# Kernel tuning notes

Measured on AMD Instinct MI355X. Metric: run time of the kernel, lower is better.

Reference implementation:

```python
import jax, jax.numpy as jnp
import numpy as np

N = 100000
E = 3200000
D = 64  # in_feats == hidden_feats == 64 (hardcoded in module)


def setup_inputs() -> dict:
    key = jax.random.key(0)
    ks = jax.random.split(key, 12)
    s = 1.0 / np.sqrt(D)
    return {
        "x": jax.random.normal(ks[0], (N, D), dtype=jnp.float32),
        "edge_index": jax.random.randint(ks[1], (2, E), 0, N, dtype=jnp.int64),
        "W1": jax.random.uniform(ks[2], (D, D), jnp.float32, -s, s),
        "b1": jnp.zeros((D,), jnp.float32),
        "W2": jax.random.uniform(ks[3], (D, D), jnp.float32, -s, s),
        "b2": jnp.zeros((D,), jnp.float32),
        "Wq": jax.random.uniform(ks[4], (D, D), jnp.float32, -s, s),
        "bq": jax.random.uniform(ks[5], (D,), jnp.float32, -s, s),
        "Wk": jax.random.uniform(ks[6], (D, D), jnp.float32, -s, s),
        "bk": jax.random.uniform(ks[7], (D,), jnp.float32, -s, s),
        "Wv": jax.random.uniform(ks[8], (D, D), jnp.float32, -s, s),
        "bv": jax.random.uniform(ks[9], (D,), jnp.float32, -s, s),
    }


def gcn_conv(x, src, dst, deg_inv_sqrt, W, b):
    # PyG GCNConv: linear -> normalized scatter-add over edges (self-loops included in src/dst)
    h = x @ W  # [N, D]
    norm = deg_inv_sqrt[src] * deg_inv_sqrt[dst]  # [E+N]
    msg = h[src] * norm[:, None]  # gather + scale
    out = jax.ops.segment_sum(msg, dst, num_segments=x.shape[0])  # scatter-add
    return out + b


def reference(x, edge_index, W1, b1, W2, b2, Wq, bq, Wk, bk, Wv, bv):
    n = x.shape[0]
    loop = jnp.arange(n, dtype=edge_index.dtype)
    src = jnp.concatenate([edge_index[0], loop])
    dst = jnp.concatenate([edge_index[1], loop])
    deg = jax.ops.segment_sum(jnp.ones_like(src, dtype=x.dtype), dst, num_segments=n)
    deg_inv_sqrt = jnp.where(deg > 0, jax.lax.rsqrt(deg), 0.0)

    h = jax.nn.relu(gcn_conv(x, src, dst, deg_inv_sqrt, W1, b1))
    # dropout with training=False -> identity; F.relu(relu(h)) == relu(h)
    h = jax.nn.relu(gcn_conv(h, src, dst, deg_inv_sqrt, W2, b2))

    # Attention with seq_len == 1
    q = h @ Wq + bq  # [N, D]
    k = h @ Wk + bk
    v = h @ Wv + bv
    scores = jnp.sum(q * k, axis=-1, keepdims=True)[:, :, None]  # [N,1,1]
    att = jax.nn.softmax(scores, axis=-1)  # == 1 for seq_len 1, kept for faithfulness
    context = att * v[:, None, :]  # [N,1,D]
    return context
```

## Files before the change

kernel.cpp:

```cpp
#include <hip/hip_runtime.h>
#include <hip/hip_bf16.h>
#include <cstdint>
#include <cstddef>


#define BN_SHIFT 8
#define BN 256
#define NBK 512
#define PCHUNK 4096
#define PCAP 16
#define BCAP 10240

static __device__ __forceinline__ uint32_t f32_to_bf16_bits(float f) {
    uint32_t u = __builtin_bit_cast(uint32_t, f);
    u += 0x7fffu + ((u >> 16) & 1u);
    return u >> 16;
}

static __device__ __forceinline__ void add_bf16x8(float* acc, uint4 q) {
    uint32_t w0 = q.x, w1 = q.y, w2 = q.z, w3 = q.w;
    acc[0] += __builtin_bit_cast(float, w0 << 16);
    acc[1] += __builtin_bit_cast(float, w0 & 0xffff0000u);
    acc[2] += __builtin_bit_cast(float, w1 << 16);
    acc[3] += __builtin_bit_cast(float, w1 & 0xffff0000u);
    acc[4] += __builtin_bit_cast(float, w2 << 16);
    acc[5] += __builtin_bit_cast(float, w2 & 0xffff0000u);
    acc[6] += __builtin_bit_cast(float, w3 << 16);
    acc[7] += __builtin_bit_cast(float, w3 & 0xffff0000u);
}

__global__ __launch_bounds__(256) void hist_kernel(const int* __restrict__ ei,
                                                   int* __restrict__ pcnt, int E) {
    __shared__ int lc[NBK];
    int tid = threadIdx.x;
    lc[tid] = 0; lc[tid + 256] = 0;
    __syncthreads();

    int e0 = blockIdx.x * PCHUNK;
    int m = min(PCHUNK, E - e0);
    const int* dsts = ei + E + e0;
    if ((((uintptr_t)dsts) & 15) == 0) {
        int m4 = m >> 2;
        for (int t = tid; t < m4; t += 256) {
            int4 d = ((const int4*)dsts)[t];
            atomicAdd(&lc[d.x >> BN_SHIFT], 1);
            atomicAdd(&lc[d.y >> BN_SHIFT], 1);
            atomicAdd(&lc[d.z >> BN_SHIFT], 1);
            atomicAdd(&lc[d.w >> BN_SHIFT], 1);
        }
        for (int i = (m4 << 2) + tid; i < m; i += 256)
            atomicAdd(&lc[dsts[i] >> BN_SHIFT], 1);
    } else {
        for (int i = tid; i < m; i += 256)
            atomicAdd(&lc[dsts[i] >> BN_SHIFT], 1);
    }
    __syncthreads();
    int* row = pcnt + (size_t)blockIdx.x * NBK;
    row[tid] = lc[tid];
    row[tid + 256] = lc[tid + 256];
}

__global__ __launch_bounds__(256) void pscan_kernel(int* __restrict__ pcnt,
                                                    int* __restrict__ bcnt, int PB) {
    __shared__ int ss[256];
    int b = blockIdx.x;
    int tid = threadIdx.x;
    int iper = (PB + 255) >> 8;
    int i0 = tid * iper;
    int i1 = min(PB, i0 + iper);
    int vals[8];
    int s = 0;
    for (int i = i0, k = 0; i < i1; ++i, ++k) {
        vals[k] = pcnt[(size_t)i * NBK + b];
        s += vals[k];
    }
    ss[tid] = s;
    __syncthreads();
    for (int o = 1; o < 256; o <<= 1) {
        int u = (tid >= o) ? ss[tid - o] : 0;
        __syncthreads();
        ss[tid] += u;
        __syncthreads();
    }
    int run = ss[tid] - s;
    for (int i = i0, k = 0; i < i1; ++i, ++k) {
        pcnt[(size_t)i * NBK + b] = run;
        run += vals[k];
    }
    if (tid == 255) bcnt[b] = ss[255];
}

__global__ __launch_bounds__(256) void bscan_kernel(const int* __restrict__ bcnt,
                                                    int* __restrict__ bbase) {
    __shared__ int s[256];
    int t = threadIdx.x;
    int c0 = bcnt[2 * t], c1 = bcnt[2 * t + 1];
    int v = c0 + c1;
    s[t] = v;
    __syncthreads();
    for (int off = 1; off < 256; off <<= 1) {
        int u = (t >= off) ? s[t - off] : 0;
        __syncthreads();
        s[t] += u;
        __syncthreads();
    }
    int ex = s[t] - v;
    bbase[2 * t] = ex;
    bbase[2 * t + 1] = ex + c0;
    if (t == 255) bbase[NBK] = ex + c0 + c1;
}

__global__ __launch_bounds__(256) void part_kernel(const int* __restrict__ ei,
                                                   const int* __restrict__ bbase,
                                                   const int* __restrict__ poff,
                                                   uint32_t* __restrict__ stage, int E) {
    __shared__ int cnt[NBK];
    __shared__ int base[NBK];
    __shared__ uint32_t bins[NBK * PCAP];
    int tid = threadIdx.x;
    cnt[tid] = 0; cnt[tid + 256] = 0;
    {
        const int* prow = poff + (size_t)blockIdx.x * NBK;
        base[tid] = bbase[tid] + prow[tid];
        base[tid + 256] = bbase[tid + 256] + prow[tid + 256];
    }
    __syncthreads();

    int e0 = blockIdx.x * PCHUNK;
#pragma unroll
    for (int k = 0; k < PCHUNK / 256; ++k) {
        int e = e0 + (k << 8) + tid;
        if (e < E) {
            int s = ei[e];
            int d = ei[E + e];
            int b = d >> BN_SHIFT;
            uint32_t pack = (uint32_t)s | ((uint32_t)(d & (BN - 1)) << 17);
            int pos = atomicAdd(&cnt[b], 1);
            if (pos < PCAP) bins[b * PCAP + pos] = pack;
            else stage[base[b] + pos] = pack;
        }
    }
    __syncthreads();

    int wave = tid >> 6, lane = tid & 63;
    int sub = lane >> 4, idx = lane & 15;
    for (int b0 = wave * 4; b0 < NBK; b0 += 16) {
        int b = b0 + sub;
        int c = min(cnt[b], PCAP);
        if (idx < c) stage[base[b] + idx] = bins[b * PCAP + idx];
    }
}

__global__ __launch_bounds__(256) void build_kernel(const uint32_t* __restrict__ stage,
                                                    const int* __restrict__ bbase,
                                                    int* __restrict__ rowptr,
                                                    float* __restrict__ dis,
                                                    int* __restrict__ col, int n) {
    __shared__ uint32_t eb[BCAP];
    __shared__ int cnt[BN];
    __shared__ int off[BN];
    __shared__ int cur[BN];
    __shared__ int ssum[256];
    int tid = threadIdx.x;
    int b = blockIdx.x;
    int node0 = b << BN_SHIFT;
    int ebase = bbase[b];
    int ecnt = bbase[b + 1] - ebase;
    int colbase = ebase + node0;

    cnt[tid] = 0;
    cur[tid] = 0;
    __syncthreads();

    bool fits = (ecnt <= BCAP);
    for (int i = tid; i < ecnt; i += 256) {
        uint32_t pk = stage[ebase + i];
        if (fits) eb[i] = pk;
        atomicAdd(&cnt[pk >> 17], 1);
    }
    __syncthreads();

    int c = cnt[tid] + 1;
    ssum[tid] = c;
    __syncthreads();
    for (int o = 1; o < 256; o <<= 1) {
        int u = (tid >= o) ? ssum[tid - o] : 0;
        __syncthreads();
        ssum[tid] += u;
        __syncthreads();
    }
    int ex = ssum[tid] - c;
    off[tid] = ex;
    int node = node0 + tid;
    if (node <= n) rowptr[node] = colbase + ex;
    if (node < n) {
        dis[node] = rsqrtf((float)c);
        col[colbase + ex] = node << 7;
    }
    __syncthreads();

    if (fits) {
        for (int i = tid; i < ecnt; i += 256) {
            uint32_t pk = eb[i];
            int doff = pk >> 17;
            int p = atomicAdd(&cur[doff], 1);
            col[colbase + off[doff] + 1 + p] = (int)(pk & 0x1ffff) << 7;
        }
    } else {
        for (int i = tid; i < ecnt; i += 256) {
            uint32_t pk = stage[ebase + i];
            int doff = pk >> 17;
            int p = atomicAdd(&cur[doff], 1);
            col[colbase + off[doff] + 1 + p] = (int)(pk & 0x1ffff) << 7;
        }
    }
}

template <int MODE>
__global__ __launch_bounds__(256) void gemm_kernel(const float* __restrict__ x,
                                                   const float* __restrict__ W,
                                                   const float* __restrict__ dis,
                                                   const float* __restrict__ bias,
                                                   void* __restrict__ out, int n) {
    __shared__ float Wl[64 * 64];
    int t = threadIdx.x;
    {
        const float4* W4 = (const float4*)W;
        float4* Wl4 = (float4*)Wl;
#pragma unroll
        for (int i = 0; i < 4; ++i) Wl4[t + i * 256] = W4[t + i * 256];
    }
    __syncthreads();

    int row = blockIdx.x * 256 + t;
    if (row >= n) return;

    const float4* xr = (const float4*)(x + (size_t)row * 64);
    float4 acc4[16];
#pragma unroll
    for (int p = 0; p < 16; ++p) acc4[p] = make_float4(0.f, 0.f, 0.f, 0.f);

    float4 xq = xr[0];
    for (int k4 = 0; k4 < 16; ++k4) {
        float4 xn = xq;
        if (k4 < 15) xn = xr[k4 + 1];
        float xs[4] = {xq.x, xq.y, xq.z, xq.w};
#pragma unroll
        for (int kk = 0; kk < 4; ++kk) {
            float xk = xs[kk];
            const float4* wr = (const float4*)&Wl[((k4 << 2) + kk) << 6];
#pragma unroll
            for (int j4 = 0; j4 < 16; ++j4) {
                float4 wv = wr[j4];
                acc4[j4].x = fmaf(xk, wv.x, acc4[j4].x);
                acc4[j4].y = fmaf(xk, wv.y, acc4[j4].y);
                acc4[j4].z = fmaf(xk, wv.z, acc4[j4].z);
                acc4[j4].w = fmaf(xk, wv.w, acc4[j4].w);
            }
        }
        xq = xn;
    }

    if (MODE == 0) {
        float s = dis[row];
        uint4* go = (uint4*)out;
#pragma unroll
        for (int p = 0; p < 8; ++p) {
            float4 a = acc4[2 * p];
            float4 bq = acc4[2 * p + 1];
            uint4 o;
            o.x = (f32_to_bf16_bits(a.y * s) << 16) | f32_to_bf16_bits(a.x * s);
            o.y = (f32_to_bf16_bits(a.w * s) << 16) | f32_to_bf16_bits(a.z * s);
            o.z = (f32_to_bf16_bits(bq.y * s) << 16) | f32_to_bf16_bits(bq.x * s);
            o.w = (f32_to_bf16_bits(bq.w * s) << 16) | f32_to_bf16_bits(bq.z * s);
            go[(size_t)row * 8 + p] = o;
        }
    } else {
        const float4* b4 = (const float4*)bias;
        float4* fo = (float4*)out;
#pragma unroll
        for (int p = 0; p < 16; ++p) {
            float4 bb = b4[p];
            float4 a = acc4[p];
            a.x += bb.x; a.y += bb.y; a.z += bb.z; a.w += bb.w;
            fo[(size_t)row * 16 + p] = a;
        }
    }
}

__global__ __launch_bounds__(256) void agg_kernel(const char* __restrict__ g,
                                                  const int* __restrict__ rowptr,
                                                  const int* __restrict__ col,
                                                  const float* __restrict__ dis,
                                                  const float* __restrict__ bias,
                                                  float* __restrict__ out, int n) {
    int wid = (blockIdx.x * 256 + threadIdx.x) >> 6;
    if (wid >= n) return;
    int lane = threadIdx.x & 63;
    int grp = lane >> 3;
    int chk16 = (lane & 7) << 4;

    float acc[8];
#pragma unroll
    for (int j = 0; j < 8; ++j) acc[j] = 0.f;

    int beg = rowptr[wid];
    int end = rowptr[wid + 1];
    int e = beg + grp;
    for (; e + 8 < end; e += 16) {
        int o0 = col[e] + chk16;
        int o1 = col[e + 8] + chk16;
        uint4 q0 = *(const uint4*)(g + o0);
        uint4 q1 = *(const uint4*)(g + o1);
        add_bf16x8(acc, q0);
        add_bf16x8(acc, q1);
    }
    if (e < end) {
        int o = col[e] + chk16;
        add_bf16x8(acc, *(const uint4*)(g + o));
    }

#pragma unroll
    for (int m = 8; m < 64; m <<= 1) {
#pragma unroll
        for (int j = 0; j < 8; ++j) acc[j] += __shfl_xor(acc[j], m, 64);
    }

    float dv = dis[wid];
    float v = acc[0];
#pragma unroll
    for (int j = 1; j < 8; ++j) v = (grp == j) ? acc[j] : v;
    int f = (chk16 >> 1) + grp;
    v = fmaxf(fmaf(v, dv, bias[f]), 0.f);
    out[(size_t)wid * 64 + f] = v;
}

extern "C" void kernel_launch(void* const* d_in, const int* in_sizes, int n_in,
                              void* d_out, int out_size, void* d_ws, size_t ws_size,
                              hipStream_t stream) {
    const float* x  = (const float*)d_in[0];
    const int*   ei = (const int*)d_in[1];
    const float* W1 = (const float*)d_in[2];
    const float* b1 = (const float*)d_in[3];
    const float* W2 = (const float*)d_in[4];
    const float* b2 = (const float*)d_in[5];
    const float* Wv = (const float*)d_in[10];
    const float* bv = (const float*)d_in[11];

    const int N = in_sizes[0] / 64;
    const int E = in_sizes[1] / 2;
    const int NB = (N + BN - 1) >> BN_SHIFT;
    const int PB = (E + PCHUNK - 1) / PCHUNK;

    auto align_up = [](size_t v) { return (v + 255) & ~(size_t)255; };
    char* p = (char*)d_ws;
    int*   rowptr = (int*)p;    p += align_up((size_t)(N + 1) * 4);
    float* dis    = (float*)p;  p += align_up((size_t)N * 4);
    int*   pcnt   = (int*)p;    p += align_up((size_t)PB * NBK * 4);
    int*   bcnt   = (int*)p;    p += align_up((size_t)NBK * 4);
    int*   bbase  = (int*)p;    p += align_up((size_t)(NBK + 1) * 4);
    int*   col    = (int*)p;    p += align_up((size_t)(E + N + BN) * 4);
    size_t gsz    = (size_t)N * 128 > (size_t)E * 4 ? (size_t)N * 128 : (size_t)E * 4;
    char*  gbuf   = p;          p += align_up(gsz);
    float* xbuf   = (float*)p;  p += align_up((size_t)N * 256);
    uint32_t* stage = (uint32_t*)gbuf;

    int nbl = (N + 255) / 256;
    int abl = (N + 3) / 4;

    hist_kernel<<<PB, 256, 0, stream>>>(ei, pcnt, E);
    pscan_kernel<<<NBK, 256, 0, stream>>>(pcnt, bcnt, PB);
    bscan_kernel<<<1, 256, 0, stream>>>(bcnt, bbase);
    part_kernel<<<PB, 256, 0, stream>>>(ei, bbase, pcnt, stage, E);
    build_kernel<<<NB, 256, 0, stream>>>(stage, bbase, rowptr, dis, col, N);

    gemm_kernel<0><<<nbl, 256, 0, stream>>>(x, W1, dis, nullptr, gbuf, N);
    agg_kernel<<<abl, 256, 0, stream>>>(gbuf, rowptr, col, dis, b1, xbuf, N);

    gemm_kernel<0><<<nbl, 256, 0, stream>>>(xbuf, W2, dis, nullptr, gbuf, N);
    agg_kernel<<<abl, 256, 0, stream>>>(gbuf, rowptr, col, dis, b2, xbuf, N);

    gemm_kernel<1><<<nbl, 256, 0, stream>>>(xbuf, Wv, nullptr, bv, d_out, N);
}
```

Before: 350.8 us.

## Map one 8-lane group per node in aggregation and fold block scan into consumers

The aggregation kernel now assigns each node to an 8-lane group that walks all of its edges serially, instead of spreading a node's edges across a full wave. This removes the cross-lane shuffle reduction and lets each wave hold eight nodes' gathers in flight, and outputs are written as float4. Separately, the single-block bucket scan kernel is removed and the scan is recomputed redundantly inside each partition and build block, saving one launch at the cost of extra per-block work. Lanes may sit idle when node degrees differ within a wave.

```diff
diff --git a/kernel.cpp b/kernel.cpp
--- a/kernel.cpp
+++ b/kernel.cpp
@@ -27,6 +27,26 @@
     acc[5] += __builtin_bit_cast(float, w2 & 0xffff0000u);
     acc[6] += __builtin_bit_cast(float, w3 << 16);
     acc[7] += __builtin_bit_cast(float, w3 & 0xffff0000u);
+}
+
+static __device__ __forceinline__ void scan_bcnt(const int* __restrict__ bcnt,
+                                                 int* sbb, int* ssum) {
+    int t = threadIdx.x;
+    int c0 = bcnt[2 * t], c1 = bcnt[2 * t + 1];
+    int v = c0 + c1;
+    ssum[t] = v;
+    __syncthreads();
+    for (int o = 1; o < 256; o <<= 1) {
+        int u = (t >= o) ? ssum[t - o] : 0;
+        __syncthreads();
+        ssum[t] += u;
+        __syncthreads();
+    }
+    int ex = ssum[t] - v;
+    sbb[2 * t] = ex;
+    sbb[2 * t + 1] = ex + c0;
+    if (t == 255) sbb[NBK] = ex + c0 + c1;
+    __syncthreads();
 }
 
 __global__ __launch_bounds__(256) void hist_kernel(const int* __restrict__ ei,
@@ -90,39 +110,23 @@
     if (tid == 255) bcnt[b] = ss[255];
 }
 
-__global__ __launch_bounds__(256) void bscan_kernel(const int* __restrict__ bcnt,
-                                                    int* __restrict__ bbase) {
-    __shared__ int s[256];
-    int t = threadIdx.x;
-    int c0 = bcnt[2 * t], c1 = bcnt[2 * t + 1];
-    int v = c0 + c1;
-    s[t] = v;
-    __syncthreads();
-    for (int off = 1; off < 256; off <<= 1) {
-        int u = (t >= off) ? s[t - off] : 0;
-        __syncthreads();
-        s[t] += u;
-        __syncthreads();
-    }
-    int ex = s[t] - v;
-    bbase[2 * t] = ex;
-    bbase[2 * t + 1] = ex + c0;
-    if (t == 255) bbase[NBK] = ex + c0 + c1;
-}
-
 __global__ __launch_bounds__(256) void part_kernel(const int* __restrict__ ei,
-                                                   const int* __restrict__ bbase,
+                                                   const int* __restrict__ bcnt,
                                                    const int* __restrict__ poff,
                                                    uint32_t* __restrict__ stage, int E) {
+    __shared__ int sbb[NBK + 1];
+    __shared__ int ssum[256];
     __shared__ int cnt[NBK];
     __shared__ int base[NBK];
     __shared__ uint32_t bins[NBK * PCAP];
     int tid = threadIdx.x;
+    scan_bcnt(bcnt, sbb, ssum);
+
     cnt[tid] = 0; cnt[tid + 256] = 0;
     {
         const int* prow = poff + (size_t)blockIdx.x * NBK;
-        base[tid] = bbase[tid] + prow[tid];
-        base[tid + 256] = bbase[tid + 256] + prow[tid + 256];
+        base[tid] = sbb[tid] + prow[tid];
+        base[tid + 256] = sbb[tid + 256] + prow[tid + 256];
     }
     __syncthreads();
 
@@ -152,20 +156,22 @@
 }
 
 __global__ __launch_bounds__(256) void build_kernel(const uint32_t* __restrict__ stage,
-                                                    const int* __restrict__ bbase,
+                                                    const int* __restrict__ bcnt,
                                                     int* __restrict__ rowptr,
                                                     float* __restrict__ dis,
                                                     int* __restrict__ col, int n) {
+    __shared__ int sbb[NBK + 1];
     __shared__ uint32_t eb[BCAP];
     __shared__ int cnt[BN];
     __shared__ int off[BN];
     __shared__ int cur[BN];
     __shared__ int ssum[256];
     int tid = threadIdx.x;
+    scan_bcnt(bcnt, sbb, ssum);
     int b = blockIdx.x;
     int node0 = b << BN_SHIFT;
-    int ebase = bbase[b];
-    int ecnt = bbase[b + 1] - ebase;
+    int ebase = sbb[b];
+    int ecnt = sbb[b + 1] - ebase;
     int colbase = ebase + node0;
 
     cnt[tid] = 0;
@@ -294,45 +300,45 @@
                                                   const float* __restrict__ dis,
                                                   const float* __restrict__ bias,
                                                   float* __restrict__ out, int n) {
-    int wid = (blockIdx.x * 256 + threadIdx.x) >> 6;
-    if (wid >= n) return;
-    int lane = threadIdx.x & 63;
-    int grp = lane >> 3;
-    int chk16 = (lane & 7) << 4;
+    int tid = threadIdx.x;
+    int wave = tid >> 6, lane = tid & 63;
+    int grp = lane >> 3, chk = lane & 7;
+    int node = blockIdx.x * 32 + (wave << 3) + grp;
+    if (node >= n) return;
+
+    const char* gc = g + (chk << 4);
 
     float acc[8];
 #pragma unroll
     for (int j = 0; j < 8; ++j) acc[j] = 0.f;
 
-    int beg = rowptr[wid];
-    int end = rowptr[wid + 1];
-    int e = beg + grp;
-    for (; e + 8 < end; e += 16) {
-        int o0 = col[e] + chk16;
-        int o1 = col[e + 8] + chk16;
-        uint4 q0 = *(const uint4*)(g + o0);
-        uint4 q1 = *(const uint4*)(g + o1);
+    int e = rowptr[node];
+    int end = rowptr[node + 1];
+    for (; e + 1 < end; e += 2) {
+        int o0 = col[e];
+        int o1 = col[e + 1];
+        uint4 q0 = *(const uint4*)(gc + o0);
+        uint4 q1 = *(const uint4*)(gc + o1);
         add_bf16x8(acc, q0);
         add_bf16x8(acc, q1);
     }
-    if (e < end) {
-        int o = col[e] + chk16;
-        add_bf16x8(acc, *(const uint4*)(g + o));
-    }
-
-#pragma unroll
-    for (int m = 8; m < 64; m <<= 1) {
-#pragma unroll
-        for (int j = 0; j < 8; ++j) acc[j] += __shfl_xor(acc[j], m, 64);
-    }
-
-    float dv = dis[wid];
-    float v = acc[0];
-#pragma unroll
-    for (int j = 1; j < 8; ++j) v = (grp == j) ? acc[j] : v;
-    int f = (chk16 >> 1) + grp;
-    v = fmaxf(fmaf(v, dv, bias[f]), 0.f);
-    out[(size_t)wid * 64 + f] = v;
+    if (e < end) add_bf16x8(acc, *(const uint4*)(gc + col[e]));
+
+    float dv = dis[node];
+    const float4* b4 = (const float4*)bias;
+    float4 bb0 = b4[chk * 2], bb1 = b4[chk * 2 + 1];
+    float4 o0, o1;
+    o0.x = fmaxf(fmaf(acc[0], dv, bb0.x), 0.f);
+    o0.y = fmaxf(fmaf(acc[1], dv, bb0.y), 0.f);
+    o0.z = fmaxf(fmaf(acc[2], dv, bb0.z), 0.f);
+    o0.w = fmaxf(fmaf(acc[3], dv, bb0.w), 0.f);
+    o1.x = fmaxf(fmaf(acc[4], dv, bb1.x), 0.f);
+    o1.y = fmaxf(fmaf(acc[5], dv, bb1.y), 0.f);
+    o1.z = fmaxf(fmaf(acc[6], dv, bb1.z), 0.f);
+    o1.w = fmaxf(fmaf(acc[7], dv, bb1.w), 0.f);
+    float4* fo = (float4*)(out + (size_t)node * 64 + (chk << 3));
+    fo[0] = o0;
+    fo[1] = o1;
 }
 
 extern "C" void kernel_launch(void* const* d_in, const int* in_sizes, int n_in,
@@ -358,7 +364,6 @@
     float* dis    = (float*)p;  p += align_up((size_t)N * 4);
     int*   pcnt   = (int*)p;    p += align_up((size_t)PB * NBK * 4);
     int*   bcnt   = (int*)p;    p += align_up((size_t)NBK * 4);
-    int*   bbase  = (int*)p;    p += align_up((size_t)(NBK + 1) * 4);
     int*   col    = (int*)p;    p += align_up((size_t)(E + N + BN) * 4);
     size_t gsz    = (size_t)N * 128 > (size_t)E * 4 ? (size_t)N * 128 : (size_t)E * 4;
     char*  gbuf   = p;          p += align_up(gsz);
@@ -366,13 +371,12 @@
     uint32_t* stage = (uint32_t*)gbuf;
 
     int nbl = (N + 255) / 256;
-    int abl = (N + 3) / 4;
-
-    hist_kernel<<<PB, 256, 0, stream>>>(ei, pcnt, E);
+    int abl = (N + 31) / 32;
+
+    hist_kernel <<<PB, 256, 0, stream>>>(ei, pcnt, E);
     pscan_kernel<<<NBK, 256, 0, stream>>>(pcnt, bcnt, PB);
-    bscan_kernel<<<1, 256, 0, stream>>>(bcnt, bbase);
-    part_kernel<<<PB, 256, 0, stream>>>(ei, bbase, pcnt, stage, E);
-    build_kernel<<<NB, 256, 0, stream>>>(stage, bbase, rowptr, dis, col, N);
+    part_kernel <<<PB, 256, 0, stream>>>(ei, bcnt, pcnt, stage, E);
+    build_kernel<<<NB, 256, 0, stream>>>(stage, bcnt, rowptr, dis, col, N);
 
     gemm_kernel<0><<<nbl, 256, 0, stream>>>(x, W1, dis, nullptr, gbuf, N);
     agg_kernel<<<abl, 256, 0, stream>>>(gbuf, rowptr, col, dis, b1, xbuf, N);
```

After: 367.2 us. 1.05x slower.
